# Optimization experiments

Measured on AMD Instinct MI355X. Metric: run time of the kernel, lower is better.

## Reference

```python
import jax, jax.numpy as jnp
import numpy as np

N_HEADS = 8
D_K = 256
SCALE = D_K ** -0.5


def setup_inputs() -> dict:
    key = jax.random.key(0)
    k1, k2, k3 = jax.random.split(key, 3)
    B, C, H, W = 8, 256, 32, 32
    x = jax.random.normal(k1, (B, C, H, W), dtype=jnp.float32)
    Wp = jax.random.normal(k2, (C, N_HEADS * D_K * 3), dtype=jnp.float32) * (C ** -0.5)
    bp = jnp.zeros((N_HEADS * D_K * 3,), dtype=jnp.float32)
    Wo = jax.random.normal(k3, (N_HEADS * D_K, C), dtype=jnp.float32) * ((N_HEADS * D_K) ** -0.5)
    bo = jnp.zeros((C,), dtype=jnp.float32)
    return {"x": x, "Wp": Wp, "bp": bp, "Wo": Wo, "bo": bo}


def reference(x, Wp, bp, Wo, bo):
    B, C, H, W = x.shape
    S = H * W
    # [B,C,H,W] -> [B,S,C] tokens
    xt = x.reshape(B, C, S).transpose(0, 2, 1)
    qkv = (xt @ Wp + bp).reshape(B, S, N_HEADS, 3 * D_K)
    q, k, v = jnp.split(qkv, 3, axis=-1)  # each [B,S,H,dk]
    attn = jnp.einsum('bihd,bjhd->bijh', q, k) * SCALE
    attn = jax.nn.softmax(attn, axis=2)  # over j (keys)
    res = jnp.einsum('bijh,bjhd->bihd', attn, v).reshape(B, S, N_HEADS * D_K)
    res = res @ Wo + bo + xt  # residual
    return res.transpose(0, 2, 1).reshape(B, C, H, W)
```

## Files before the change

kernel.cpp:

```cpp
#include <hip/hip_runtime.h>

#define NH    8
#define DK    256
#define SS    1024
#define QSCALE 0.09016844136947155f
#define TSH   8192

using frag8  = __attribute__((ext_vector_type(8))) short;
using f32x4  = __attribute__((ext_vector_type(4))) float;
using f32x16 = __attribute__((ext_vector_type(16))) float;

__device__ __forceinline__ unsigned short f2bf(float f) {
    unsigned int u = __float_as_uint(f);
    return (unsigned short)((u + 0x7FFFu + ((u >> 16) & 1u)) >> 16);
}
__device__ __forceinline__ unsigned int pk2bf(float lo, float hi) {
    unsigned int ul = __float_as_uint(lo), uh = __float_as_uint(hi);
    ul += 0x7FFFu + ((ul >> 16) & 1u);
    uh += 0x7FFFu + ((uh >> 16) & 1u);
    return (ul >> 16) | (uh & 0xFFFF0000u);
}

__device__ __forceinline__ void load_lds16(const void* g, void* l) {
    __builtin_amdgcn_global_load_lds(
        (const __attribute__((address_space(1))) unsigned int*)g,
        (__attribute__((address_space(3))) unsigned int*)l, 16, 0, 0);
}


__global__ __launch_bounds__(256) void k0_all(
    const float* __restrict__ x,  unsigned short* __restrict__ xb,
    const float* __restrict__ Wp, unsigned short* __restrict__ Wpt,
    const float* __restrict__ Wo, unsigned short* __restrict__ Wot)
{
    __shared__ float tile[32][33];
    const int bid = blockIdx.x;
    const float* in; unsigned short* out; int R, C, c0, r0;
    if (bid < 2048) {
        int rr = bid;
        in = x + (size_t)(rr >> 8) * 256 * 1024;
        out = xb + (size_t)(rr >> 8) * 256 * 1024;
        R = 256; C = 1024; c0 = (rr & 31) * 32; r0 = ((rr >> 5) & 7) * 32;
    } else if (bid < 3584) {
        int rr = bid - 2048;
        in = Wp; out = Wpt; R = 256; C = 6144;
        c0 = (rr % 192) * 32; r0 = (rr / 192) * 32;
    } else {
        int rr = bid - 3584;
        in = Wo; out = Wot; R = 2048; C = 256;
        c0 = (rr & 7) * 32; r0 = (rr >> 3) * 32;
    }
    const int tx = threadIdx.x & 31, ty = threadIdx.x >> 5;
#pragma unroll
    for (int j = 0; j < 4; j++)
        tile[ty + j * 8][tx] = in[(size_t)(r0 + ty + j * 8) * C + c0 + tx];
    __syncthreads();
#pragma unroll
    for (int j = 0; j < 4; j++)
        out[(size_t)(c0 + ty + j * 8) * R + r0 + tx] = f2bf(tile[tx][ty + j * 8]);
}

__global__ __launch_bounds__(256) void k1_qkv(
    const unsigned short* __restrict__ xb, const unsigned short* __restrict__ Wpt,
    const float* __restrict__ bp,
    unsigned short* __restrict__ qb, unsigned short* __restrict__ kb,
    unsigned short* __restrict__ vb)
{
    __shared__ unsigned short As[128 * 32];
    __shared__ unsigned short Bs[128 * 32];
    const int t = threadIdx.x;
    const int wave = t >> 6, lane = t & 63;
    const int quad = lane >> 4, l16 = lane & 15;
    const int n0 = blockIdx.x * 128, m0 = blockIdx.y * 128;
    const int b = m0 >> 10, s0 = m0 & 1023;
    const int mq = (wave >> 1) * 64, nq = (wave & 1) * 64;
    const int lr = lane >> 2, lc = (lane & 3) * 8;

    const unsigned short* Ag = xb + (size_t)(b * 1024 + s0) * 256;
    const unsigned short* Bg = Wpt + (size_t)n0 * 256;

    f32x4 acc[4][4];
#pragma unroll
    for (int i = 0; i < 4; i++)
#pragma unroll
        for (int j = 0; j < 4; j++) acc[i][j] = (f32x4){0.f, 0.f, 0.f, 0.f};

    for (int k0 = 0; k0 < 256; k0 += 32) {
#pragma unroll
        for (int j = 0; j < 2; j++) {
            int ch = wave + j * 4;
            load_lds16(Ag + (size_t)(ch * 16 + lr) * 256 + k0 + lc, &As[ch * 512]);
            load_lds16(Bg + (size_t)(ch * 16 + lr) * 256 + k0 + lc, &Bs[ch * 512]);
        }
        __syncthreads();
        frag8 af[4], bf[4];
#pragma unroll
        for (int i = 0; i < 4; i++)
            af[i] = *(const frag8*)(&As[(mq + i * 16 + l16) * 32 + quad * 8]);
#pragma unroll
        for (int j = 0; j < 4; j++)
            bf[j] = *(const frag8*)(&Bs[(nq + j * 16 + l16) * 32 + quad * 8]);
#pragma unroll
        for (int i = 0; i < 4; i++)
#pragma unroll
            for (int j = 0; j < 4; j++)
                acc[i][j] = __builtin_amdgcn_mfma_f32_16x16x32_bf16(af[i], bf[j], acc[i][j], 0, 0, 0);
        __syncthreads();
    }

    const int h = n0 / 768;
    const int rem = n0 - h * 768;
    const int tt = rem >> 8;
    const int dbase = (rem & 255) + nq;
    const size_t bh = (size_t)(b * NH + h);
    float bias[4];
#pragma unroll
    for (int j = 0; j < 4; j++) bias[j] = bp[n0 + nq + j * 16 + l16];

    if (tt < 2) {
        const float sc = (tt == 0) ? QSCALE : 1.0f;
        unsigned short* dst = (tt == 0 ? qb : kb) + bh * 32 * TSH;
#pragma unroll
        for (int i = 0; i < 4; i++)
#pragma unroll
            for (int r = 0; r < 4; r++) {
                int s = s0 + mq + i * 16 + quad * 4 + r;
                const size_t tb = (size_t)(s >> 5) * TSH + (s & 31) * 8;
#pragma unroll
                for (int j = 0; j < 4; j++) {
                    int d = dbase + j * 16 + l16;
                    dst[tb + (d >> 3) * 256 + (d & 7)] = f2bf((acc[i][j][r] + bias[j]) * sc);
                }
            }
    } else {
        unsigned short* dst = vb + bh * 32 * TSH;
        const int chunk = ((quad & 1)) * 2048;
        const int jjb = (quad & 2) * 2;
#pragma unroll
        for (int j = 0; j < 4; j++) {
            int d = dbase + j * 16 + l16;
#pragma unroll
            for (int i = 0; i < 4; i++) {
                int g = ((mq >> 4) + i) & 1;
                size_t tile = (size_t)((s0 + mq + i * 16) >> 5) * TSH;
                uint2 st;
                st.x = pk2bf(acc[i][j][0] + bias[j], acc[i][j][1] + bias[j]);
                st.y = pk2bf(acc[i][j][2] + bias[j], acc[i][j][3] + bias[j]);
                *(uint2*)(&dst[tile + g * 4096 + chunk + d * 8 + jjb]) = st;
            }
        }
    }
}

__global__ __launch_bounds__(256, 2) void k2_attn(
    const unsigned short* __restrict__ qb, const unsigned short* __restrict__ kb,
    const unsigned short* __restrict__ vb, unsigned short* __restrict__ ob)
{
    __shared__ unsigned short Ks[2][TSH];
    __shared__ unsigned short Vs[2][TSH];

    const int t = threadIdx.x;
    const int wave = t >> 6, lane = t & 63;
    const int l32 = lane & 31, hw = lane >> 5;

    const int flat = blockIdx.x;
    const int xcd = flat & 7, tt2 = flat >> 3;
    const int qt = tt2 & 7;
    const int bh = xcd * 8 + (tt2 >> 3);

    const int qrow0 = qt * 128 + wave * 32;

    frag8 qf[16];
    {
        const unsigned short* qp = qb + ((size_t)bh * 32 + qt * 4 + wave) * TSH
                                 + hw * 256 + l32 * 8;
#pragma unroll
        for (int s = 0; s < 16; s++) qf[s] = *(const frag8*)(qp + s * 512);
    }

    f32x16 acc[8];
#pragma unroll
    for (int nb = 0; nb < 8; nb++)
#pragma unroll
        for (int r = 0; r < 16; r++) acc[nb][r] = 0.f;
    float lsum = 0.f;

    const unsigned short* kt0 = kb + (size_t)bh * 32 * TSH;
    const unsigned short* vt0 = vb + (size_t)bh * 32 * TSH;

#pragma unroll
    for (int j = 0; j < 4; j++) {
        int c = wave * 4 + j;
        load_lds16(kt0 + c * 512 + lane * 8, &Ks[0][c * 512]);
        load_lds16(vt0 + c * 512 + lane * 8, &Vs[0][c * 512]);
    }
    __syncthreads();

    for (int kt = 0; kt < 32; kt++) {
        const int cur = kt & 1;

        if (kt < 31) {
            const unsigned short* kg = kt0 + (size_t)(kt + 1) * TSH;
            const unsigned short* vg = vt0 + (size_t)(kt + 1) * TSH;
#pragma unroll
            for (int j = 0; j < 4; j++) {
                int c = wave * 4 + j;
                load_lds16(kg + c * 512 + lane * 8, &Ks[cur ^ 1][c * 512]);
                load_lds16(vg + c * 512 + lane * 8, &Vs[cur ^ 1][c * 512]);
            }
        }

        f32x16 sa0, sa1;
#pragma unroll
        for (int r = 0; r < 16; r++) { sa0[r] = 0.f; sa1[r] = 0.f; }
#pragma unroll
        for (int s = 0; s < 16; s += 2) {
            frag8 kf0 = *(const frag8*)(&Ks[cur][(2 * s + hw) * 256 + l32 * 8]);
            frag8 kf1 = *(const frag8*)(&Ks[cur][(2 * s + 2 + hw) * 256 + l32 * 8]);
            sa0 = __builtin_amdgcn_mfma_f32_32x32x16_bf16(kf0, qf[s], sa0, 0, 0, 0);
            sa1 = __builtin_amdgcn_mfma_f32_32x32x16_bf16(kf1, qf[s + 1], sa1, 0, 0, 0);
        }

        float p[16];
#pragma unroll
        for (int e = 0; e < 16; e++) {
            p[e] = exp2f(sa0[e] + sa1[e]);
            lsum += p[e];
        }
        frag8 pf[2];
#pragma unroll
        for (int g = 0; g < 2; g++) {
            uint4 w;
            w.x = pk2bf(p[g * 8 + 0], p[g * 8 + 1]);
            w.y = pk2bf(p[g * 8 + 2], p[g * 8 + 3]);
            w.z = pk2bf(p[g * 8 + 4], p[g * 8 + 5]);
            w.w = pk2bf(p[g * 8 + 6], p[g * 8 + 7]);
            pf[g] = *(frag8*)&w;
        }

#pragma unroll
        for (int g = 0; g < 2; g++)
#pragma unroll
            for (int nb = 0; nb < 8; nb++) {
                frag8 vf = *(const frag8*)(&Vs[cur][(g * 2 + hw) * 2048 + (nb * 32 + l32) * 8]);
                acc[nb] = __builtin_amdgcn_mfma_f32_32x32x16_bf16(pf[g], vf, acc[nb], 0, 0, 0);
            }

        __syncthreads();
    }

    lsum += __shfl_xor(lsum, 32);
    const float linv = 1.f / lsum;

    unsigned short* og = ob + ((size_t)bh * SS + qrow0) * DK + l32;
#pragma unroll
    for (int r = 0; r < 16; r++) {
        const int rowl = (r & 3) + 8 * (r >> 2) + 4 * hw;
        const float li = __shfl(linv, rowl, 64);
        unsigned short* orow = og + (size_t)rowl * DK;
#pragma unroll
        for (int nb = 0; nb < 8; nb++)
            orow[nb * 32] = f2bf(acc[nb][r] * li);
    }
}

__global__ __launch_bounds__(256) void k3_proj(
    const unsigned short* __restrict__ ob, const unsigned short* __restrict__ Wot,
    const float* __restrict__ bo, const float* __restrict__ x,
    float* __restrict__ out)
{
    __shared__ unsigned short As[2][2048];
    __shared__ unsigned short Bs[2][2048];
    const int t = threadIdx.x;
    const int wave = t >> 6, lane = t & 63;
    const int quad = lane >> 4, l16 = lane & 15;
    const int n0 = blockIdx.x * 64, m0 = blockIdx.y * 64;
    const int b = m0 >> 10, s0 = m0 & 1023;
    const int mq = (wave >> 1) * 32, nq = (wave & 1) * 32;
    const int lr = lane >> 2, lc = (lane & 3) * 8;

    const unsigned short* Bg = Wot + (size_t)n0 * 2048;

    f32x4 acc[2][2];
#pragma unroll
    for (int i = 0; i < 2; i++)
#pragma unroll
        for (int j = 0; j < 2; j++) acc[i][j] = (f32x4){0.f, 0.f, 0.f, 0.f};

    for (int k0 = 0; k0 < 2048; k0 += 64) {
        const int h = k0 >> 8, d0 = k0 & 255;
        const unsigned short* Ag = ob + (size_t)((b * 8 + h) * 1024 + s0) * 256 + d0;
#pragma unroll
        for (int sl = 0; sl < 2; sl++) {
            load_lds16(Ag + (size_t)(wave * 16 + lr) * 256 + sl * 32 + lc, &As[sl][wave * 512]);
            load_lds16(Bg + (size_t)(wave * 16 + lr) * 2048 + k0 + sl * 32 + lc, &Bs[sl][wave * 512]);
        }
        __syncthreads();
#pragma unroll
        for (int sl = 0; sl < 2; sl++) {
            frag8 af[2], bf[2];
#pragma unroll
            for (int i = 0; i < 2; i++)
                af[i] = *(const frag8*)(&As[sl][(mq + i * 16 + l16) * 32 + quad * 8]);
#pragma unroll
            for (int j = 0; j < 2; j++)
                bf[j] = *(const frag8*)(&Bs[sl][(nq + j * 16 + l16) * 32 + quad * 8]);
#pragma unroll
            for (int i = 0; i < 2; i++)
#pragma unroll
                for (int j = 0; j < 2; j++)
                    acc[i][j] = __builtin_amdgcn_mfma_f32_16x16x32_bf16(af[i], bf[j], acc[i][j], 0, 0, 0);
        }
        __syncthreads();
    }

#pragma unroll
    for (int j = 0; j < 2; j++) {
        int c = n0 + nq + j * 16 + l16;
        float bias = bo[c];
#pragma unroll
        for (int i = 0; i < 2; i++) {
            int s = s0 + mq + i * 16 + quad * 4;
            size_t off = (size_t)(b * 256 + c) * 1024 + s;
            float4 xv = *(const float4*)(&x[off]);
            float4 ov;
            ov.x = acc[i][j][0] + bias + xv.x;
            ov.y = acc[i][j][1] + bias + xv.y;
            ov.z = acc[i][j][2] + bias + xv.z;
            ov.w = acc[i][j][3] + bias + xv.w;
            *(float4*)(&out[off]) = ov;
        }
    }
}

extern "C" void kernel_launch(void* const* d_in, const int* in_sizes, int n_in,
                              void* d_out, int out_size, void* d_ws, size_t ws_size,
                              hipStream_t stream)
{
    const float* x  = (const float*)d_in[0];
    const float* Wp = (const float*)d_in[1];
    const float* bp = (const float*)d_in[2];
    const float* Wo = (const float*)d_in[3];
    const float* bo = (const float*)d_in[4];
    float* out = (float*)d_out;

    char* ws = (char*)d_ws;
    unsigned short* qb  = (unsigned short*)(ws);
    unsigned short* kb  = (unsigned short*)(ws + 33554432);
    unsigned short* vb  = (unsigned short*)(ws + 67108864);
    unsigned short* xb  = (unsigned short*)(ws + 100663296);
    unsigned short* Wpt = (unsigned short*)(ws + 104857600);
    unsigned short* Wot = (unsigned short*)(ws + 108003328);

    k0_all<<<dim3(4096), 256, 0, stream>>>(x, xb, Wp, Wpt, Wo, Wot);
    k1_qkv<<<dim3(48, 64), 256, 0, stream>>>(xb, Wpt, bp, qb, kb, vb);
    k2_attn<<<dim3(512), 256, 0, stream>>>(qb, kb, vb, qb );
    k3_proj<<<dim3(4, 128), 256, 0, stream>>>(qb, Wot, bo, x, out);
}
```

Baseline: 225.0 us.

## Double-buffer LDS in QKV and projection GEMMs, transpose Q/K epilogue stores

Both the QKV and output-projection GEMMs now use two LDS buffers, so the next K-tile loads while MFMAs run on the current one, with a single barrier per iteration. For Q/K tiles the QKV kernel swaps the MFMA operand roles so accumulator rows follow the head dimension. This allows packed 8-byte stores and float4 bias loads in the tiled Q/K layout, replacing scattered 2-byte stores. The cost is doubled LDS use, which may lower occupancy.

Result: faster. 218.3 us (-3.0%).

```diff
diff --git a/kernel.cpp b/kernel.cpp
--- a/kernel.cpp
+++ b/kernel.cpp
@@ -66,8 +66,8 @@
     unsigned short* __restrict__ qb, unsigned short* __restrict__ kb,
     unsigned short* __restrict__ vb)
 {
-    __shared__ unsigned short As[128 * 32];
-    __shared__ unsigned short Bs[128 * 32];
+    __shared__ unsigned short As[2][128 * 32];
+    __shared__ unsigned short Bs[2][128 * 32];
     const int t = threadIdx.x;
     const int wave = t >> 6, lane = t & 63;
     const int quad = lane >> 4, l16 = lane & 15;
@@ -76,6 +76,10 @@
     const int mq = (wave >> 1) * 64, nq = (wave & 1) * 64;
     const int lr = lane >> 2, lc = (lane & 3) * 8;
 
+    const int h = n0 / 768;
+    const int rem = n0 - h * 768;
+    const int tt = rem >> 8;
+
     const unsigned short* Ag = xb + (size_t)(b * 1024 + s0) * 256;
     const unsigned short* Bg = Wpt + (size_t)n0 * 256;
 
@@ -85,21 +89,34 @@
 #pragma unroll
         for (int j = 0; j < 4; j++) acc[i][j] = (f32x4){0.f, 0.f, 0.f, 0.f};
 
-    for (int k0 = 0; k0 < 256; k0 += 32) {
-#pragma unroll
-        for (int j = 0; j < 2; j++) {
-            int ch = wave + j * 4;
-            load_lds16(Ag + (size_t)(ch * 16 + lr) * 256 + k0 + lc, &As[ch * 512]);
-            load_lds16(Bg + (size_t)(ch * 16 + lr) * 256 + k0 + lc, &Bs[ch * 512]);
-        }
-        __syncthreads();
+#pragma unroll
+    for (int j = 0; j < 2; j++) {
+        int ch = wave + j * 4;
+        load_lds16(Ag + (size_t)(ch * 16 + lr) * 256 + lc, &As[0][ch * 512]);
+        load_lds16(Bg + (size_t)(ch * 16 + lr) * 256 + lc, &Bs[0][ch * 512]);
+    }
+    __syncthreads();
+
+    for (int kt = 0; kt < 8; kt++) {
+        const int cur = kt & 1;
+        if (kt < 7) {
+            const int k0 = (kt + 1) * 32;
+#pragma unroll
+            for (int j = 0; j < 2; j++) {
+                int ch = wave + j * 4;
+                load_lds16(Ag + (size_t)(ch * 16 + lr) * 256 + k0 + lc, &As[cur ^ 1][ch * 512]);
+                load_lds16(Bg + (size_t)(ch * 16 + lr) * 256 + k0 + lc, &Bs[cur ^ 1][ch * 512]);
+            }
+        }
+        const unsigned short* Fa = (tt < 2) ? &Bs[cur][0] : &As[cur][0];
+        const unsigned short* Fb = (tt < 2) ? &As[cur][0] : &Bs[cur][0];
         frag8 af[4], bf[4];
 #pragma unroll
         for (int i = 0; i < 4; i++)
-            af[i] = *(const frag8*)(&As[(mq + i * 16 + l16) * 32 + quad * 8]);
+            af[i] = *(const frag8*)(&Fa[(mq + i * 16 + l16) * 32 + quad * 8]);
 #pragma unroll
         for (int j = 0; j < 4; j++)
-            bf[j] = *(const frag8*)(&Bs[(nq + j * 16 + l16) * 32 + quad * 8]);
+            bf[j] = *(const frag8*)(&Fb[(nq + j * 16 + l16) * 32 + quad * 8]);
 #pragma unroll
         for (int i = 0; i < 4; i++)
 #pragma unroll
@@ -108,37 +125,39 @@
         __syncthreads();
     }
 
-    const int h = n0 / 768;
-    const int rem = n0 - h * 768;
-    const int tt = rem >> 8;
-    const int dbase = (rem & 255) + nq;
+    const int dcol0 = rem & 255;
     const size_t bh = (size_t)(b * NH + h);
-    float bias[4];
-#pragma unroll
-    for (int j = 0; j < 4; j++) bias[j] = bp[n0 + nq + j * 16 + l16];
 
     if (tt < 2) {
         const float sc = (tt == 0) ? QSCALE : 1.0f;
         unsigned short* dst = (tt == 0 ? qb : kb) + bh * 32 * TSH;
 #pragma unroll
-        for (int i = 0; i < 4; i++)
-#pragma unroll
-            for (int r = 0; r < 4; r++) {
-                int s = s0 + mq + i * 16 + quad * 4 + r;
-                const size_t tb = (size_t)(s >> 5) * TSH + (s & 31) * 8;
-#pragma unroll
-                for (int j = 0; j < 4; j++) {
-                    int d = dbase + j * 16 + l16;
-                    dst[tb + (d >> 3) * 256 + (d & 7)] = f2bf((acc[i][j][r] + bias[j]) * sc);
-                }
-            }
+        for (int i = 0; i < 4; i++) {
+            const int mloc = mq + i * 16;
+            float4 b4 = *(const float4*)(&bp[n0 + mloc + quad * 4]);
+            const int octet = ((dcol0 + mloc) >> 3) + (quad >> 1);
+            const int drem4 = (quad & 1) * 4;
+#pragma unroll
+            for (int j = 0; j < 4; j++) {
+                const int s = s0 + nq + j * 16 + l16;
+                unsigned short* cell = dst + (size_t)(s >> 5) * TSH
+                                     + octet * 256 + (s & 31) * 8 + drem4;
+                uint2 st;
+                st.x = pk2bf((acc[i][j][0] + b4.x) * sc, (acc[i][j][1] + b4.y) * sc);
+                st.y = pk2bf((acc[i][j][2] + b4.z) * sc, (acc[i][j][3] + b4.w) * sc);
+                *(uint2*)cell = st;
+            }
+        }
     } else {
         unsigned short* dst = vb + bh * 32 * TSH;
-        const int chunk = ((quad & 1)) * 2048;
+        const int chunk = (quad & 1) * 2048;
         const int jjb = (quad & 2) * 2;
+        float bias[4];
+#pragma unroll
+        for (int j = 0; j < 4; j++) bias[j] = bp[n0 + nq + j * 16 + l16];
 #pragma unroll
         for (int j = 0; j < 4; j++) {
-            int d = dbase + j * 16 + l16;
+            int d = dcol0 + nq + j * 16 + l16;
 #pragma unroll
             for (int i = 0; i < 4; i++) {
                 int g = ((mq >> 4) + i) & 1;
@@ -269,8 +288,8 @@
     const float* __restrict__ bo, const float* __restrict__ x,
     float* __restrict__ out)
 {
-    __shared__ unsigned short As[2][2048];
-    __shared__ unsigned short Bs[2][2048];
+    __shared__ unsigned short As[2][2][2048];
+    __shared__ unsigned short Bs[2][2][2048];
     const int t = threadIdx.x;
     const int wave = t >> 6, lane = t & 63;
     const int quad = lane >> 4, l16 = lane & 15;
@@ -287,24 +306,32 @@
 #pragma unroll
         for (int j = 0; j < 2; j++) acc[i][j] = (f32x4){0.f, 0.f, 0.f, 0.f};
 
-    for (int k0 = 0; k0 < 2048; k0 += 64) {
+    auto stage = [&](int buf, int kt) {
+        const int k0 = kt * 64;
         const int h = k0 >> 8, d0 = k0 & 255;
         const unsigned short* Ag = ob + (size_t)((b * 8 + h) * 1024 + s0) * 256 + d0;
 #pragma unroll
         for (int sl = 0; sl < 2; sl++) {
-            load_lds16(Ag + (size_t)(wave * 16 + lr) * 256 + sl * 32 + lc, &As[sl][wave * 512]);
-            load_lds16(Bg + (size_t)(wave * 16 + lr) * 2048 + k0 + sl * 32 + lc, &Bs[sl][wave * 512]);
-        }
-        __syncthreads();
+            load_lds16(Ag + (size_t)(wave * 16 + lr) * 256 + sl * 32 + lc, &As[buf][sl][wave * 512]);
+            load_lds16(Bg + (size_t)(wave * 16 + lr) * 2048 + k0 + sl * 32 + lc, &Bs[buf][sl][wave * 512]);
+        }
+    };
+
+    stage(0, 0);
+    __syncthreads();
+
+    for (int kt = 0; kt < 32; kt++) {
+        const int cur = kt & 1;
+        if (kt < 31) stage(cur ^ 1, kt + 1);
 #pragma unroll
         for (int sl = 0; sl < 2; sl++) {
             frag8 af[2], bf[2];
 #pragma unroll
             for (int i = 0; i < 2; i++)
-                af[i] = *(const frag8*)(&As[sl][(mq + i * 16 + l16) * 32 + quad * 8]);
+                af[i] = *(const frag8*)(&As[cur][sl][(mq + i * 16 + l16) * 32 + quad * 8]);
 #pragma unroll
             for (int j = 0; j < 2; j++)
-                bf[j] = *(const frag8*)(&Bs[sl][(nq + j * 16 + l16) * 32 + quad * 8]);
+                bf[j] = *(const frag8*)(&Bs[cur][sl][(nq + j * 16 + l16) * 32 + quad * 8]);
 #pragma unroll
             for (int i = 0; i < 2; i++)
 #pragma unroll
```

## Switch all GEMMs to MFMA-fragment panel layouts with 32x32 MFMA and double buffering

Applied to the files above, without the earlier changes.

The prep kernel now writes x, Wp and Wo in a tiled panel layout that matches the 32x32x16 MFMA fragment order. That lets the QKV and output-projection GEMMs stage whole contiguous panels into double-buffered LDS with direct global-to-LDS loads. The attention kernel swaps MFMA operand order so its output is transposed, and it writes O in the same panel layout with packed stores instead of scattered scalar ones. The projection kernel uses larger M tiles, but its epilogue now does scalar, partly strided reads and writes of x and out, which may cost bandwidth.

New measurement: 225.3 us. About the same (+0.1%).

```diff
diff --git a/kernel.cpp b/kernel.cpp
--- a/kernel.cpp
+++ b/kernel.cpp
@@ -7,7 +7,6 @@
 #define TSH   8192
 
 using frag8  = __attribute__((ext_vector_type(8))) short;
-using f32x4  = __attribute__((ext_vector_type(4))) float;
 using f32x16 = __attribute__((ext_vector_type(16))) float;
 
 __device__ __forceinline__ unsigned short f2bf(float f) {
@@ -29,124 +28,136 @@
 
 
 __global__ __launch_bounds__(256) void k0_all(
-    const float* __restrict__ x,  unsigned short* __restrict__ xb,
-    const float* __restrict__ Wp, unsigned short* __restrict__ Wpt,
-    const float* __restrict__ Wo, unsigned short* __restrict__ Wot)
+    const float* __restrict__ x,  unsigned short* __restrict__ xbT,
+    const float* __restrict__ Wp, unsigned short* __restrict__ WptT,
+    const float* __restrict__ Wo, unsigned short* __restrict__ WotT)
 {
     __shared__ float tile[32][33];
     const int bid = blockIdx.x;
-    const float* in; unsigned short* out; int R, C, c0, r0;
+    const float* in; unsigned short* outp; int C, c0, r0; size_t pbase; int psz;
     if (bid < 2048) {
         int rr = bid;
-        in = x + (size_t)(rr >> 8) * 256 * 1024;
-        out = xb + (size_t)(rr >> 8) * 256 * 1024;
-        R = 256; C = 1024; c0 = (rr & 31) * 32; r0 = ((rr >> 5) & 7) * 32;
+        int b = rr >> 8;
+        in = x + (size_t)b * 256 * 1024;
+        C = 1024; c0 = (rr & 31) * 32; r0 = ((rr >> 5) & 7) * 32;
+        psz = 8192; pbase = (size_t)(b * 32 + (c0 >> 5)); outp = xbT;
     } else if (bid < 3584) {
         int rr = bid - 2048;
-        in = Wp; out = Wpt; R = 256; C = 6144;
-        c0 = (rr % 192) * 32; r0 = (rr / 192) * 32;
+        in = Wp; C = 6144; c0 = (rr % 192) * 32; r0 = (rr / 192) * 32;
+        psz = 8192; pbase = (size_t)(c0 >> 5); outp = WptT;
     } else {
         int rr = bid - 3584;
-        in = Wo; out = Wot; R = 2048; C = 256;
-        c0 = (rr & 7) * 32; r0 = (rr >> 3) * 32;
+        in = Wo; C = 256; c0 = (rr & 7) * 32; r0 = (rr >> 3) * 32;
+        psz = 65536; pbase = (size_t)(c0 >> 5); outp = WotT;
     }
     const int tx = threadIdx.x & 31, ty = threadIdx.x >> 5;
 #pragma unroll
     for (int j = 0; j < 4; j++)
         tile[ty + j * 8][tx] = in[(size_t)(r0 + ty + j * 8) * C + c0 + tx];
     __syncthreads();
+    const int k = r0 + tx;
+    unsigned short* dst = outp + pbase * psz + ((k >> 3) * 32) * 8 + (k & 7);
 #pragma unroll
     for (int j = 0; j < 4; j++)
-        out[(size_t)(c0 + ty + j * 8) * R + r0 + tx] = f2bf(tile[tx][ty + j * 8]);
+        dst[(ty + j * 8) * 8] = f2bf(tile[tx][ty + j * 8]);
 }
 
 __global__ __launch_bounds__(256) void k1_qkv(
-    const unsigned short* __restrict__ xb, const unsigned short* __restrict__ Wpt,
+    const unsigned short* __restrict__ xbT, const unsigned short* __restrict__ WptT,
     const float* __restrict__ bp,
     unsigned short* __restrict__ qb, unsigned short* __restrict__ kb,
     unsigned short* __restrict__ vb)
 {
-    __shared__ unsigned short As[128 * 32];
-    __shared__ unsigned short Bs[128 * 32];
+    __shared__ unsigned short Xs[2][4096];
+    __shared__ unsigned short Ws[2][4096];
     const int t = threadIdx.x;
     const int wave = t >> 6, lane = t & 63;
-    const int quad = lane >> 4, l16 = lane & 15;
+    const int l32 = lane & 31, hw = lane >> 5;
     const int n0 = blockIdx.x * 128, m0 = blockIdx.y * 128;
     const int b = m0 >> 10, s0 = m0 & 1023;
-    const int mq = (wave >> 1) * 64, nq = (wave & 1) * 64;
-    const int lr = lane >> 2, lc = (lane & 3) * 8;
-
-    const unsigned short* Ag = xb + (size_t)(b * 1024 + s0) * 256;
-    const unsigned short* Bg = Wpt + (size_t)n0 * 256;
-
-    f32x4 acc[4][4];
-#pragma unroll
-    for (int i = 0; i < 4; i++)
-#pragma unroll
-        for (int j = 0; j < 4; j++) acc[i][j] = (f32x4){0.f, 0.f, 0.f, 0.f};
-
-    for (int k0 = 0; k0 < 256; k0 += 32) {
-#pragma unroll
-        for (int j = 0; j < 2; j++) {
-            int ch = wave + j * 4;
-            load_lds16(Ag + (size_t)(ch * 16 + lr) * 256 + k0 + lc, &As[ch * 512]);
-            load_lds16(Bg + (size_t)(ch * 16 + lr) * 256 + k0 + lc, &Bs[ch * 512]);
-        }
-        __syncthreads();
-        frag8 af[4], bf[4];
-#pragma unroll
-        for (int i = 0; i < 4; i++)
-            af[i] = *(const frag8*)(&As[(mq + i * 16 + l16) * 32 + quad * 8]);
-#pragma unroll
-        for (int j = 0; j < 4; j++)
-            bf[j] = *(const frag8*)(&Bs[(nq + j * 16 + l16) * 32 + quad * 8]);
-#pragma unroll
-        for (int i = 0; i < 4; i++)
-#pragma unroll
-            for (int j = 0; j < 4; j++)
-                acc[i][j] = __builtin_amdgcn_mfma_f32_16x16x32_bf16(af[i], bf[j], acc[i][j], 0, 0, 0);
-        __syncthreads();
-    }
 
     const int h = n0 / 768;
     const int rem = n0 - h * 768;
     const int tt = rem >> 8;
-    const int dbase = (rem & 255) + nq;
-    const size_t bh = (size_t)(b * NH + h);
-    float bias[4];
-#pragma unroll
-    for (int j = 0; j < 4; j++) bias[j] = bp[n0 + nq + j * 16 + l16];
+    const int dcol0 = rem & 255;
+
+    const unsigned short* Xg = xbT + (size_t)(b * 32 + (s0 >> 5)) * TSH;
+    const unsigned short* Wg = WptT + (size_t)(n0 >> 5) * TSH;
+
+    f32x16 acc[4];
+#pragma unroll
+    for (int j = 0; j < 4; j++)
+#pragma unroll
+        for (int r = 0; r < 16; r++) acc[j][r] = 0.f;
+
+    auto stage = [&](int buf, int kt) {
+#pragma unroll
+        for (int j = 0; j < 4; j++) {
+            int rgn = wave * 4 + j;
+            if (rgn < 8) {
+                int p = rgn >> 1, half = rgn & 1;
+                load_lds16(Xg + (size_t)p * TSH + kt * 1024 + half * 512 + lane * 8,
+                           &Xs[buf][p * 1024 + half * 512]);
+            } else {
+                int r2 = rgn - 8, p = r2 >> 1, half = r2 & 1;
+                load_lds16(Wg + (size_t)p * TSH + kt * 1024 + half * 512 + lane * 8,
+                           &Ws[buf][p * 1024 + half * 512]);
+            }
+        }
+    };
+
+    stage(0, 0);
+    __syncthreads();
+
+    for (int kt = 0; kt < 8; kt++) {
+        const int cur = kt & 1;
+        if (kt < 7) stage(cur ^ 1, kt + 1);
+        const unsigned short* Fa = (tt < 2) ? &Ws[cur][wave * 1024] : &Xs[cur][wave * 1024];
+        const unsigned short* Fb = (tt < 2) ? &Xs[cur][0] : &Ws[cur][0];
+#pragma unroll
+        for (int t2 = 0; t2 < 2; t2++) {
+            frag8 af = *(const frag8*)(Fa + (2 * t2 + hw) * 256 + l32 * 8);
+#pragma unroll
+            for (int j = 0; j < 4; j++) {
+                frag8 bf = *(const frag8*)(Fb + j * 1024 + (2 * t2 + hw) * 256 + l32 * 8);
+                acc[j] = __builtin_amdgcn_mfma_f32_32x32x16_bf16(af, bf, acc[j], 0, 0, 0);
+            }
+        }
+        __syncthreads();
+    }
 
     if (tt < 2) {
         const float sc = (tt == 0) ? QSCALE : 1.0f;
-        unsigned short* dst = (tt == 0 ? qb : kb) + bh * 32 * TSH;
-#pragma unroll
-        for (int i = 0; i < 4; i++)
-#pragma unroll
-            for (int r = 0; r < 4; r++) {
-                int s = s0 + mq + i * 16 + quad * 4 + r;
-                const size_t tb = (size_t)(s >> 5) * TSH + (s & 31) * 8;
-#pragma unroll
-                for (int j = 0; j < 4; j++) {
-                    int d = dbase + j * 16 + l16;
-                    dst[tb + (d >> 3) * 256 + (d & 7)] = f2bf((acc[i][j][r] + bias[j]) * sc);
-                }
-            }
+        unsigned short* dst0 = (tt == 0 ? qb : kb);
+        const int dc0 = (dcol0 + wave * 32) >> 3;
+#pragma unroll
+        for (int G = 0; G < 4; G++) {
+            float4 bb = *(const float4*)(&bp[n0 + wave * 32 + 4 * hw + 8 * G]);
+#pragma unroll
+            for (int j = 0; j < 4; j++) {
+                unsigned short* cell = dst0
+                    + (size_t)((b * NH + h) * 32 + (s0 >> 5) + j) * TSH
+                    + ((dc0 + G) * 32 + l32) * 8 + 4 * hw;
+                uint2 st;
+                st.x = pk2bf((acc[j][4 * G + 0] + bb.x) * sc, (acc[j][4 * G + 1] + bb.y) * sc);
+                st.y = pk2bf((acc[j][4 * G + 2] + bb.z) * sc, (acc[j][4 * G + 3] + bb.w) * sc);
+                *(uint2*)cell = st;
+            }
+        }
     } else {
-        unsigned short* dst = vb + bh * 32 * TSH;
-        const int chunk = ((quad & 1)) * 2048;
-        const int jjb = (quad & 2) * 2;
+        unsigned short* vt = vb + (size_t)((b * NH + h) * 32 + (s0 >> 5) + wave) * TSH;
 #pragma unroll
         for (int j = 0; j < 4; j++) {
-            int d = dbase + j * 16 + l16;
-#pragma unroll
-            for (int i = 0; i < 4; i++) {
-                int g = ((mq >> 4) + i) & 1;
-                size_t tile = (size_t)((s0 + mq + i * 16) >> 5) * TSH;
+            const int d = dcol0 + j * 32 + l32;
+            const float bv = bp[n0 + j * 32 + l32];
+#pragma unroll
+            for (int G = 0; G < 4; G++) {
+                int g = G >> 1;
+                unsigned short* cell = vt + (g * 2 + hw) * 2048 + d * 8 + 4 * (G & 1);
                 uint2 st;
-                st.x = pk2bf(acc[i][j][0] + bias[j], acc[i][j][1] + bias[j]);
-                st.y = pk2bf(acc[i][j][2] + bias[j], acc[i][j][3] + bias[j]);
-                *(uint2*)(&dst[tile + g * 4096 + chunk + d * 8 + jjb]) = st;
+                st.x = pk2bf(acc[j][4 * G + 0] + bv, acc[j][4 * G + 1] + bv);
+                st.y = pk2bf(acc[j][4 * G + 2] + bv, acc[j][4 * G + 3] + bv);
+                *(uint2*)cell = st;
             }
         }
     }
@@ -167,8 +178,6 @@
     const int xcd = flat & 7, tt2 = flat >> 3;
     const int qt = tt2 & 7;
     const int bh = xcd * 8 + (tt2 >> 3);
-
-    const int qrow0 = qt * 128 + wave * 32;
 
     frag8 qf[16];
     {
@@ -243,92 +252,99 @@
 #pragma unroll
             for (int nb = 0; nb < 8; nb++) {
                 frag8 vf = *(const frag8*)(&Vs[cur][(g * 2 + hw) * 2048 + (nb * 32 + l32) * 8]);
-                acc[nb] = __builtin_amdgcn_mfma_f32_32x32x16_bf16(pf[g], vf, acc[nb], 0, 0, 0);
+                acc[nb] = __builtin_amdgcn_mfma_f32_32x32x16_bf16(vf, pf[g], acc[nb], 0, 0, 0);
             }
 
         __syncthreads();
     }
 
     lsum += __shfl_xor(lsum, 32);
-    const float linv = 1.f / lsum;
-
-    unsigned short* og = ob + ((size_t)bh * SS + qrow0) * DK + l32;
-#pragma unroll
-    for (int r = 0; r < 16; r++) {
-        const int rowl = (r & 3) + 8 * (r >> 2) + 4 * hw;
-        const float li = __shfl(linv, rowl, 64);
-        unsigned short* orow = og + (size_t)rowl * DK;
-#pragma unroll
-        for (int nb = 0; nb < 8; nb++)
-            orow[nb * 32] = f2bf(acc[nb][r] * li);
-    }
+    const float li = 1.f / lsum;
+
+    unsigned short* opan = ob + ((size_t)bh * 32 + qt * 4 + wave) * TSH;
+#pragma unroll
+    for (int nb = 0; nb < 8; nb++)
+#pragma unroll
+        for (int G = 0; G < 4; G++) {
+            unsigned short* cell = opan + ((nb * 4 + G) * 32 + l32) * 8 + 4 * hw;
+            uint2 st;
+            st.x = pk2bf(acc[nb][4 * G + 0] * li, acc[nb][4 * G + 1] * li);
+            st.y = pk2bf(acc[nb][4 * G + 2] * li, acc[nb][4 * G + 3] * li);
+            *(uint2*)cell = st;
+        }
 }
 
 __global__ __launch_bounds__(256) void k3_proj(
-    const unsigned short* __restrict__ ob, const unsigned short* __restrict__ Wot,
+    const unsigned short* __restrict__ Ob, const unsigned short* __restrict__ WotT,
     const float* __restrict__ bo, const float* __restrict__ x,
     float* __restrict__ out)
 {
     __shared__ unsigned short As[2][2048];
-    __shared__ unsigned short Bs[2][2048];
+    __shared__ unsigned short Bs[2][4096];
     const int t = threadIdx.x;
     const int wave = t >> 6, lane = t & 63;
-    const int quad = lane >> 4, l16 = lane & 15;
-    const int n0 = blockIdx.x * 64, m0 = blockIdx.y * 64;
+    const int l32 = lane & 31, hw = lane >> 5;
+    const int wc = wave & 1, wt = wave >> 1;
+    const int c0 = blockIdx.x * 64, m0 = blockIdx.y * 128;
     const int b = m0 >> 10, s0 = m0 & 1023;
-    const int mq = (wave >> 1) * 32, nq = (wave & 1) * 32;
-    const int lr = lane >> 2, lc = (lane & 3) * 8;
-
-    const unsigned short* Bg = Wot + (size_t)n0 * 2048;
-
-    f32x4 acc[2][2];
-#pragma unroll
-    for (int i = 0; i < 2; i++)
-#pragma unroll
-        for (int j = 0; j < 2; j++) acc[i][j] = (f32x4){0.f, 0.f, 0.f, 0.f};
-
-    for (int k0 = 0; k0 < 2048; k0 += 64) {
-        const int h = k0 >> 8, d0 = k0 & 255;
-        const unsigned short* Ag = ob + (size_t)((b * 8 + h) * 1024 + s0) * 256 + d0;
-#pragma unroll
-        for (int sl = 0; sl < 2; sl++) {
-            load_lds16(Ag + (size_t)(wave * 16 + lr) * 256 + sl * 32 + lc, &As[sl][wave * 512]);
-            load_lds16(Bg + (size_t)(wave * 16 + lr) * 2048 + k0 + sl * 32 + lc, &Bs[sl][wave * 512]);
+
+    const unsigned short* Ag = WotT + (size_t)(c0 >> 5) * 65536;
+
+    f32x16 acc[2];
+#pragma unroll
+    for (int pp = 0; pp < 2; pp++)
+#pragma unroll
+        for (int r = 0; r < 16; r++) acc[pp][r] = 0.f;
+
+    auto stage = [&](int buf, int kt) {
+        const int hh = kt >> 3, lc = (kt & 7) * 4;
+#pragma unroll
+        for (int j = 0; j < 3; j++) {
+            int rgn = wave * 3 + j;
+            if (rgn < 4) {
+                int wp = rgn >> 1, half = rgn & 1;
+                load_lds16(Ag + (size_t)wp * 65536 + kt * 1024 + half * 512 + lane * 8,
+                           &As[buf][wp * 1024 + half * 512]);
+            } else {
+                int r2 = rgn - 4, p = r2 >> 1, half = r2 & 1;
+                load_lds16(Ob + (size_t)((b * NH + hh) * 32 + (s0 >> 5) + p) * TSH
+                               + lc * 256 + half * 512 + lane * 8,
+                           &Bs[buf][p * 1024 + half * 512]);
+            }
+        }
+    };
+
+    stage(0, 0);
+    __syncthreads();
+
+    for (int kt = 0; kt < 64; kt++) {
+        const int cur = kt & 1;
+        if (kt < 63) stage(cur ^ 1, kt + 1);
+#pragma unroll
+        for (int t2 = 0; t2 < 2; t2++) {
+            frag8 af = *(const frag8*)(&As[cur][wc * 1024 + (2 * t2 + hw) * 256 + l32 * 8]);
+#pragma unroll
+            for (int pp = 0; pp < 2; pp++) {
+                frag8 bf = *(const frag8*)(&Bs[cur][(wt * 2 + pp) * 1024 + (2 * t2 + hw) * 256 + l32 * 8]);
+                acc[pp] = __builtin_amdgcn_mfma_f32_32x32x16_bf16(af, bf, acc[pp], 0, 0, 0);
+            }
         }
         __syncthreads();
-#pragma unroll
-        for (int sl = 0; sl < 2; sl++) {
-            frag8 af[2], bf[2];
-#pragma unroll
-            for (int i = 0; i < 2; i++)
-                af[i] = *(const frag8*)(&As[sl][(mq + i * 16 + l16) * 32 + quad * 8]);
-#pragma unroll
-            for (int j = 0; j < 2; j++)
-                bf[j] = *(const frag8*)(&Bs[sl][(nq + j * 16 + l16) * 32 + quad * 8]);
-#pragma unroll
-            for (int i = 0; i < 2; i++)
-#pragma unroll
-                for (int j = 0; j < 2; j++)
-                    acc[i][j] = __builtin_amdgcn_mfma_f32_16x16x32_bf16(af[i], bf[j], acc[i][j], 0, 0, 0);
-        }
-        __syncthreads();
-    }
-
-#pragma unroll
-    for (int j = 0; j < 2; j++) {
-        int c = n0 + nq + j * 16 + l16;
-        float bias = bo[c];
-#pragma unroll
-        for (int i = 0; i < 2; i++) {
-            int s = s0 + mq + i * 16 + quad * 4;
-            size_t off = (size_t)(b * 256 + c) * 1024 + s;
-            float4 xv = *(const float4*)(&x[off]);
-            float4 ov;
-            ov.x = acc[i][j][0] + bias + xv.x;
-            ov.y = acc[i][j][1] + bias + xv.y;
-            ov.z = acc[i][j][2] + bias + xv.z;
-            ov.w = acc[i][j][3] + bias + xv.w;
-            *(float4*)(&out[off]) = ov;
+    }
+
+#pragma unroll
+    for (int G = 0; G < 4; G++) {
+        float4 bb = *(const float4*)(&bo[c0 + wc * 32 + 4 * hw + 8 * G]);
+#pragma unroll
+        for (int pp = 0; pp < 2; pp++) {
+            const int s = s0 + wt * 64 + pp * 32 + l32;
+#pragma unroll
+            for (int e = 0; e < 4; e++) {
+                const int ch = c0 + wc * 32 + 4 * hw + 8 * G + e;
+                const float bbe = (e == 0) ? bb.x : (e == 1) ? bb.y : (e == 2) ? bb.z : bb.w;
+                size_t off = (size_t)(b * 256 + ch) * 1024 + s;
+                out[off] = acc[pp][4 * G + e] + bbe + x[off];
+            }
         }
     }
 }
@@ -345,15 +361,15 @@
     float* out = (float*)d_out;
 
     char* ws = (char*)d_ws;
-    unsigned short* qb  = (unsigned short*)(ws);
-    unsigned short* kb  = (unsigned short*)(ws + 33554432);
-    unsigned short* vb  = (unsigned short*)(ws + 67108864);
-    unsigned short* xb  = (unsigned short*)(ws + 100663296);
-    unsigned short* Wpt = (unsigned short*)(ws + 104857600);
-    unsigned short* Wot = (unsigned short*)(ws + 108003328);
-
-    k0_all<<<dim3(4096), 256, 0, stream>>>(x, xb, Wp, Wpt, Wo, Wot);
-    k1_qkv<<<dim3(48, 64), 256, 0, stream>>>(xb, Wpt, bp, qb, kb, vb);
+    unsigned short* qb   = (unsigned short*)(ws);
+    unsigned short* kb   = (unsigned short*)(ws + 33554432);
+    unsigned short* vb   = (unsigned short*)(ws + 67108864);
+    unsigned short* xbT  = (unsigned short*)(ws + 100663296);
+    unsigned short* WptT = (unsigned short*)(ws + 104857600);
+    unsigned short* WotT = (unsigned short*)(ws + 108003328);
+
+    k0_all<<<dim3(4096), 256, 0, stream>>>(x, xbT, Wp, WptT, Wo, WotT);
+    k1_qkv<<<dim3(48, 64), 256, 0, stream>>>(xbT, WptT, bp, qb, kb, vb);
     k2_attn<<<dim3(512), 256, 0, stream>>>(qb, kb, vb, qb );
-    k3_proj<<<dim3(4, 128), 256, 0, stream>>>(qb, Wot, bo, x, out);
-}
+    k3_proj<<<dim3(4, 64), 256, 0, stream>>>(qb, WotT, bo, x, out);
+}
```
